# Kernel tuning notes

Hardware: AMD Instinct MI355X
Metric: run time of the kernel (lower is better)

## Reference

```python
import jax, jax.numpy as jnp
import numpy as np

TAU = 0.5
EPS = 1e-12  # torch F.normalize eps
N, HIDDEN, PROJ = 16384, 512, 128


def setup_inputs() -> dict:
    key = jax.random.key(0)
    k1, k2, k3, k4 = jax.random.split(key, 4)
    scale1 = 1.0 / np.sqrt(HIDDEN)
    scale2 = 1.0 / np.sqrt(PROJ)
    return {
        "z1": jax.random.normal(k1, (N, HIDDEN), dtype=jnp.float32),
        "z2": jax.random.normal(k2, (N, HIDDEN), dtype=jnp.float32),
        "W1": jax.random.normal(k3, (HIDDEN, PROJ), dtype=jnp.float32) * scale1,
        "b1": jnp.zeros((PROJ,), dtype=jnp.float32),
        "W2": jax.random.normal(k4, (PROJ, PROJ), dtype=jnp.float32) * scale2,
        "b2": jnp.zeros((PROJ,), dtype=jnp.float32),
    }


def _project(z, W1, b1, W2, b2):
    # GRACE projection head: Linear -> ELU -> Linear
    h = jax.nn.elu(z @ W1 + b1)
    return h @ W2 + b2


def _l2_normalize(x):
    nrm = jnp.sqrt(jnp.sum(x * x, axis=1, keepdims=True))
    return x / jnp.maximum(nrm, EPS)


def _semi_loss(u, v):
    nu = _l2_normalize(u)
    nv = _l2_normalize(v)
    intra = jnp.exp((nu @ nu.T) / TAU)  # [N, N]
    inter = jnp.exp((nu @ nv.T) / TAU)  # [N, N]
    pos = jnp.diagonal(inter)
    denom = intra.sum(axis=1) + inter.sum(axis=1) - jnp.diagonal(intra)
    return -jnp.log(pos / denom)


def reference(z1, z2, W1, b1, W2, b2):
    u = _project(z1, W1, b1, W2, b2)
    v = _project(z2, W1, b1, W2, b2)
    l1 = _semi_loss(u, v)
    l2 = _semi_loss(v, u)
    return jnp.mean((l1 + l2) * 0.5)
```

## Files before the change

### kernel.cpp

```cpp
#include <hip/hip_runtime.h>

#define NROWS 16384
#define M2    32768
#define TT    128
#define HID   512
#define PROJ  128

constexpr float SCALE_L2E = 2.8853900817779268f;
constexpr float E2        = 7.38905609893065f;

typedef float f32x2   __attribute__((ext_vector_type(2)));
typedef float f32x4   __attribute__((ext_vector_type(4)));
typedef short bf16x8  __attribute__((ext_vector_type(8)));
typedef int   i32x8   __attribute__((ext_vector_type(8)));

__device__ inline short f2bf(float x) {
  union { float f; unsigned u; } v; v.f = x;
  unsigned r = v.u + 0x7fffu + ((v.u >> 16) & 1u);
  return (short)(r >> 16);
}
__device__ inline float bf2f(short s) {
  union { unsigned u; float f; } v; v.u = ((unsigned)(unsigned short)s) << 16;
  return v.f;
}
__device__ inline unsigned char f2fp8(float x) {
  return (unsigned char)(__builtin_amdgcn_cvt_pk_fp8_f32(x, x, 0, false) & 0xff);
}
__device__ inline unsigned cvtpk_bf16(float a, float b) {
  unsigned r;
  asm("v_cvt_pk_bf16_f32 %0, %1, %2" : "=v"(r) : "v"(a), "v"(b));
  return r;
}

__global__ void kprep(const float* __restrict__ W1, const float* __restrict__ W2,
                      short* __restrict__ W1t, short* __restrict__ W2t) {
  int stride = gridDim.x * blockDim.x;
  for (int idx = blockIdx.x * blockDim.x + threadIdx.x; idx < 128 * 512; idx += stride) {
    int n = idx >> 9, k = idx & 511;
    W1t[idx] = f2bf(W1[k * 128 + n]);
  }
  for (int idx = blockIdx.x * blockDim.x + threadIdx.x; idx < 128 * 128; idx += stride) {
    int n = idx >> 7, k = idx & 127;
    W2t[idx] = f2bf(W2[k * 128 + n]);
  }
}

__global__ __launch_bounds__(256) void kproj1(const float* __restrict__ z1,
                                              const float* __restrict__ z2,
                                              const short* __restrict__ W1t,
                                              const float* __restrict__ b1,
                                              short* __restrict__ h) {
  int wave = threadIdx.x >> 6, lane = threadIdx.x & 63;
  int lr = lane & 15, lg = lane >> 4;
  const float* z = (blockIdx.x < 256) ? z1 : z2;
  int rloc = (blockIdx.x & 255) * 64 + wave * 16;
  int rglob0 = blockIdx.x * 64 + wave * 16;
  const float* zrow = z + (size_t)(rloc + lr) * HID;

  f32x4 acc[8];
#pragma unroll
  for (int ct = 0; ct < 8; ++ct) acc[ct] = (f32x4){0.f, 0.f, 0.f, 0.f};

  for (int kc = 0; kc < HID / 32; ++kc) {
    int kof = kc * 32 + lg * 8;
    f32x4 za = *(const f32x4*)(zrow + kof);
    f32x4 zb = *(const f32x4*)(zrow + kof + 4);
    union { unsigned u[4]; bf16x8 v; } af;
    af.u[0] = cvtpk_bf16(za[0], za[1]);
    af.u[1] = cvtpk_bf16(za[2], za[3]);
    af.u[2] = cvtpk_bf16(zb[0], zb[1]);
    af.u[3] = cvtpk_bf16(zb[2], zb[3]);
#pragma unroll
    for (int ct = 0; ct < 8; ++ct) {
      bf16x8 b = *(const bf16x8*)(W1t + (ct * 16 + lr) * HID + kof);
      acc[ct] = __builtin_amdgcn_mfma_f32_16x16x32_bf16(af.v, b, acc[ct], 0, 0, 0);
    }
  }
#pragma unroll
  for (int ct = 0; ct < 8; ++ct) {
    int col = ct * 16 + lr;
    float bias = b1[col];
#pragma unroll
    for (int q = 0; q < 4; ++q) {
      int row = rglob0 + lg * 4 + q;
      float x = acc[ct][q] + bias;
      x = x > 0.f ? x : expm1f(x);
      h[(size_t)row * PROJ + col] = f2bf(x);
    }
  }
}

__global__ __launch_bounds__(256) void kproj2(const short* __restrict__ h,
                                              const short* __restrict__ W2t,
                                              const float* __restrict__ b2,
                                              short* __restrict__ nn,
                                              unsigned char* __restrict__ nnf,
                                              unsigned char* __restrict__ nsf) {
  int wave = threadIdx.x >> 6, lane = threadIdx.x & 63;
  int lr = lane & 15, lg = lane >> 4;
  int row0 = blockIdx.x * 64 + wave * 16;
  const short* hrow = h + (size_t)(row0 + lr) * PROJ;

  f32x4 acc[8];
#pragma unroll
  for (int ct = 0; ct < 8; ++ct) acc[ct] = (f32x4){0.f, 0.f, 0.f, 0.f};

#pragma unroll
  for (int kc = 0; kc < PROJ / 32; ++kc) {
    int kof = kc * 32 + lg * 8;
    bf16x8 a = *(const bf16x8*)(hrow + kof);
#pragma unroll
    for (int ct = 0; ct < 8; ++ct) {
      bf16x8 b = *(const bf16x8*)(W2t + (ct * 16 + lr) * PROJ + kof);
      acc[ct] = __builtin_amdgcn_mfma_f32_16x16x32_bf16(a, b, acc[ct], 0, 0, 0);
    }
  }
#pragma unroll
  for (int ct = 0; ct < 8; ++ct) {
    float bias = b2[ct * 16 + lr];
#pragma unroll
    for (int q = 0; q < 4; ++q) acc[ct][q] += bias;
  }
  float inv[4];
#pragma unroll
  for (int q = 0; q < 4; ++q) {
    float s = 0.f;
#pragma unroll
    for (int ct = 0; ct < 8; ++ct) s += acc[ct][q] * acc[ct][q];
    s += __shfl_xor(s, 1); s += __shfl_xor(s, 2);
    s += __shfl_xor(s, 4); s += __shfl_xor(s, 8);
    inv[q] = 1.f / fmaxf(sqrtf(s), 1e-12f);
  }
#pragma unroll
  for (int ct = 0; ct < 8; ++ct) {
    int col = ct * 16 + lr;
#pragma unroll
    for (int q = 0; q < 4; ++q) {
      int row = row0 + lg * 4 + q;
      float v = acc[ct][q] * inv[q];
      nn[(size_t)row * PROJ + col]  = f2bf(v);
      nnf[(size_t)row * PROJ + col] = f2fp8(v);
      nsf[(size_t)row * PROJ + col] = f2fp8(v * SCALE_L2E);
    }
  }
}

__global__ __launch_bounds__(512, 4) void ksim11(const unsigned char* __restrict__ nnf,
                                                 const unsigned char* __restrict__ nsf,
                                                 float* __restrict__ d) {
  __shared__ long BtL[256 * 16];
  __shared__ float colbuf[8][256];

  int tid = threadIdx.x;
  int w = tid >> 6, lane = tid & 63;
  int lr = lane & 15, lg = lane >> 4;

  int t = blockIdx.x;
  float ff = (float)((2 * TT + 1) * (2 * TT + 1) - 8 * t);
  int ib = (int)(((float)(2 * TT + 1) - sqrtf(ff)) * 0.5f);
  if (ib < 0) ib = 0;
  if (ib > TT - 1) ib = TT - 1;
  while (ib > 0 && ib * (2 * TT - ib + 1) / 2 > t) --ib;
  while ((ib + 1) * (2 * TT - ib) / 2 <= t) ++ib;
  int jb = ib + (t - ib * (2 * TT - ib + 1) / 2);
  bool diag = (ib == jb);

  int i0 = ib * 256 + w * 32;

  i32x8 a[2];
#pragma unroll
  for (int rb = 0; rb < 2; ++rb)
    a[rb] = *(const i32x8*)(nsf + (size_t)(i0 + rb * 16 + lr) * PROJ + lg * 32);

  {
    int slot = tid & 15, row0 = tid >> 4;
    const long* bsrc = (const long*)(nnf + (size_t)(jb * 256 + row0) * PROJ) + slot;
    long st[8];
#pragma unroll
    for (int r = 0; r < 8; ++r) st[r] = bsrc[(size_t)r * 32 * 16];
#pragma unroll
    for (int r = 0; r < 8; ++r) {
      int row = r * 32 + row0;
      BtL[row * 16 + (slot ^ (row & 15))] = st[r];
    }
  }
  __syncthreads();

  f32x4 rs0 = (f32x4){0.f, 0.f, 0.f, 0.f};
  f32x4 rs1 = (f32x4){0.f, 0.f, 0.f, 0.f};

  const char* bb = (const char*)BtL + lr * 128;
  unsigned xo0 = (unsigned)(((lg * 4 + 0) ^ lr) << 3);
  unsigned xo1 = (unsigned)(((lg * 4 + 1) ^ lr) << 3);
  unsigned xo2 = (unsigned)(((lg * 4 + 2) ^ lr) << 3);
  unsigned xo3 = (unsigned)(((lg * 4 + 3) ^ lr) << 3);

  union BFrag { long h[4]; i32x8 v; };

  BFrag cur;
  cur.h[0] = *(const long*)(bb + xo0);
  cur.h[1] = *(const long*)(bb + xo1);
  cur.h[2] = *(const long*)(bb + xo2);
  cur.h[3] = *(const long*)(bb + xo3);

#pragma unroll 2
  for (int jt = 0; jt < 16; ++jt) {
    const char* bn = bb + 2048;
    BFrag nxt;
    nxt.h[0] = *(const long*)(bn + xo0);
    nxt.h[1] = *(const long*)(bn + xo1);
    nxt.h[2] = *(const long*)(bn + xo2);
    nxt.h[3] = *(const long*)(bn + xo3);

    f32x4 c0 = (f32x4){0.f, 0.f, 0.f, 0.f};
    f32x4 c1 = (f32x4){0.f, 0.f, 0.f, 0.f};
    c0 = __builtin_amdgcn_mfma_scale_f32_16x16x128_f8f6f4(a[0], cur.v, c0, 0, 0,
                                                          0, 0x7f7f7f7f, 0, 0x7f7f7f7f);
    c1 = __builtin_amdgcn_mfma_scale_f32_16x16x128_f8f6f4(a[1], cur.v, c1, 0, 0,
                                                          0, 0x7f7f7f7f, 0, 0x7f7f7f7f);

    f32x4 e0, e1;
#pragma unroll
    for (int q = 0; q < 4; ++q) {
      e0[q] = __builtin_amdgcn_exp2f(c0[q]);
      e1[q] = __builtin_amdgcn_exp2f(c1[q]);
    }
    rs0 += e0;
    rs1 += e1;
    f32x4 s4 = e0 + e1;
    f32x2 h2 = __builtin_shufflevector(s4, s4, 0, 1)
             + __builtin_shufflevector(s4, s4, 2, 3);
    float cs = h2[0] + h2[1];
    cs += __shfl_xor(cs, 16);
    cs += __shfl_xor(cs, 32);
    if (lg == 0) colbuf[w][jt * 16 + lr] = cs;

    cur = nxt;
    bb = bn;
  }

  float myval = 0.f;
#pragma unroll
  for (int rb = 0; rb < 2; ++rb)
#pragma unroll
    for (int q = 0; q < 4; ++q) {
      float v = (rb == 0) ? rs0[q] : rs1[q];
      v += __shfl_xor(v, 1); v += __shfl_xor(v, 2);
      v += __shfl_xor(v, 4); v += __shfl_xor(v, 8);
      if (lr == rb * 4 + q) myval = v;
    }
  if (lr < 8)
    atomicAdd(&d[i0 + (lr >> 2) * 16 + lg * 4 + (lr & 3)], myval);

  __syncthreads();
  if (!diag && tid < 256) {
    float s = 0.f;
#pragma unroll
    for (int w2 = 0; w2 < 8; ++w2) s += colbuf[w2][tid];
    atomicAdd(&d[jb * 256 + tid], s);
  }
}

__global__ __launch_bounds__(256) void kfinal(const short* __restrict__ nn,
                                              const float* __restrict__ d,
                                              float* __restrict__ out) {
  int wave = threadIdx.x >> 6, lane = threadIdx.x & 63;
  int i = blockIdx.x * 256 + threadIdx.x;

  const bf16x8* a = (const bf16x8*)(nn + (size_t)i * PROJ);
  const bf16x8* b = (const bf16x8*)(nn + (size_t)(NROWS + i) * PROJ);
  float s = 0.f;
#pragma unroll
  for (int t = 0; t < PROJ / 8; ++t) {
    bf16x8 x = a[t], y = b[t];
#pragma unroll
    for (int e = 0; e < 8; ++e) s += bf2f(x[e]) * bf2f(y[e]);
  }
  float den1 = d[i] - E2;
  float den2 = d[NROWS + i] - E2;
  float li = 0.5f * (logf(den1) + logf(den2)) - s * 2.0f;

#pragma unroll
  for (int m = 1; m < 64; m <<= 1) li += __shfl_xor(li, m);
  __shared__ float ws4[4];
  if (lane == 0) ws4[wave] = li;
  __syncthreads();
  if (threadIdx.x == 0)
    atomicAdd(out, (ws4[0] + ws4[1] + ws4[2] + ws4[3]) * (1.f / (float)NROWS));
}

extern "C" void kernel_launch(void* const* d_in, const int* in_sizes, int n_in,
                              void* d_out, int out_size, void* d_ws, size_t ws_size,
                              hipStream_t stream) {
  (void)in_sizes; (void)n_in; (void)out_size; (void)ws_size;
  const float* z1 = (const float*)d_in[0];
  const float* z2 = (const float*)d_in[1];
  const float* W1 = (const float*)d_in[2];
  const float* b1 = (const float*)d_in[3];
  const float* W2 = (const float*)d_in[4];
  const float* b2 = (const float*)d_in[5];
  float* out = (float*)d_out;

  short* W1t = (short*)d_ws;
  short* W2t = W1t + 128 * 512;
  short* hb  = W2t + 128 * 128;
  short* nn  = hb  + (size_t)M2 * PROJ;
  unsigned char* nnf = (unsigned char*)(nn + (size_t)M2 * PROJ);
  unsigned char* nsf = nnf + (size_t)M2 * PROJ;
  float* d = (float*)(nsf + (size_t)M2 * PROJ);

  hipMemsetAsync(d_out, 0, sizeof(float), stream);
  hipMemsetAsync(d, 0, (size_t)M2 * sizeof(float), stream);

  kprep<<<16, 256, 0, stream>>>(W1, W2, W1t, W2t);
  kproj1<<<M2 / 64, 256, 0, stream>>>(z1, z2, W1t, b1, hb);
  kproj2<<<M2 / 64, 256, 0, stream>>>(hb, W2t, b2, nn, nnf, nsf);
  ksim11<<<TT * (TT + 1) / 2, 512, 0, stream>>>(nnf, nsf, d);
  kfinal<<<NROWS / 256, 256, 0, stream>>>(nn, d, out);
}
```

Before: 189.1 us.

## Fuse projection kernels via LDS and interleave two column streams in sim loop

Merges the two projection GEMM kernels into one, passing the ELU hidden tile through swizzled shared memory instead of a global bf16 buffer, which removes one launch and the global round trip of the hidden activations. The similarity kernel's inner loop now processes two independent column tiles (first and second half) per iteration, doubling MFMA/exp2 independence per step to improve instruction-level parallelism. This raises register pressure in the sim kernel and adds 16KB of LDS per projection block.

```diff
diff --git a/kernel.cpp b/kernel.cpp
--- a/kernel.cpp
+++ b/kernel.cpp
@@ -45,11 +45,16 @@
   }
 }
 
-__global__ __launch_bounds__(256) void kproj1(const float* __restrict__ z1,
-                                              const float* __restrict__ z2,
-                                              const short* __restrict__ W1t,
-                                              const float* __restrict__ b1,
-                                              short* __restrict__ h) {
+__global__ __launch_bounds__(256) void kproj(const float* __restrict__ z1,
+                                             const float* __restrict__ z2,
+                                             const short* __restrict__ W1t,
+                                             const float* __restrict__ b1,
+                                             const short* __restrict__ W2t,
+                                             const float* __restrict__ b2,
+                                             short* __restrict__ nn,
+                                             unsigned char* __restrict__ nnf,
+                                             unsigned char* __restrict__ nsf) {
+  __shared__ short hls[64 * 128];
   int wave = threadIdx.x >> 6, lane = threadIdx.x & 63;
   int lr = lane & 15, lg = lane >> 4;
   const float* z = (blockIdx.x < 256) ? z1 : z2;
@@ -82,51 +87,41 @@
     float bias = b1[col];
 #pragma unroll
     for (int q = 0; q < 4; ++q) {
-      int row = rglob0 + lg * 4 + q;
+      int lrow = wave * 16 + lg * 4 + q;
       float x = acc[ct][q] + bias;
       x = x > 0.f ? x : expm1f(x);
-      h[(size_t)row * PROJ + col] = f2bf(x);
-    }
-  }
-}
-
-__global__ __launch_bounds__(256) void kproj2(const short* __restrict__ h,
-                                              const short* __restrict__ W2t,
-                                              const float* __restrict__ b2,
-                                              short* __restrict__ nn,
-                                              unsigned char* __restrict__ nnf,
-                                              unsigned char* __restrict__ nsf) {
-  int wave = threadIdx.x >> 6, lane = threadIdx.x & 63;
-  int lr = lane & 15, lg = lane >> 4;
-  int row0 = blockIdx.x * 64 + wave * 16;
-  const short* hrow = h + (size_t)(row0 + lr) * PROJ;
-
-  f32x4 acc[8];
-#pragma unroll
-  for (int ct = 0; ct < 8; ++ct) acc[ct] = (f32x4){0.f, 0.f, 0.f, 0.f};
+      int sw = (col >> 3) ^ (lrow & 15);
+      hls[lrow * 128 + sw * 8 + (col & 7)] = f2bf(x);
+    }
+  }
+  __syncthreads();
+
+  int lrow2 = wave * 16 + lr;
+  f32x4 acc2[8];
+#pragma unroll
+  for (int ct = 0; ct < 8; ++ct) acc2[ct] = (f32x4){0.f, 0.f, 0.f, 0.f};
 
 #pragma unroll
   for (int kc = 0; kc < PROJ / 32; ++kc) {
-    int kof = kc * 32 + lg * 8;
-    bf16x8 a = *(const bf16x8*)(hrow + kof);
+    bf16x8 a = *(const bf16x8*)&hls[lrow2 * 128 + (((kc * 4 + lg) ^ lr) << 3)];
 #pragma unroll
     for (int ct = 0; ct < 8; ++ct) {
-      bf16x8 b = *(const bf16x8*)(W2t + (ct * 16 + lr) * PROJ + kof);
-      acc[ct] = __builtin_amdgcn_mfma_f32_16x16x32_bf16(a, b, acc[ct], 0, 0, 0);
+      bf16x8 b = *(const bf16x8*)(W2t + (ct * 16 + lr) * PROJ + kc * 32 + lg * 8);
+      acc2[ct] = __builtin_amdgcn_mfma_f32_16x16x32_bf16(a, b, acc2[ct], 0, 0, 0);
     }
   }
 #pragma unroll
   for (int ct = 0; ct < 8; ++ct) {
     float bias = b2[ct * 16 + lr];
 #pragma unroll
-    for (int q = 0; q < 4; ++q) acc[ct][q] += bias;
+    for (int q = 0; q < 4; ++q) acc2[ct][q] += bias;
   }
   float inv[4];
 #pragma unroll
   for (int q = 0; q < 4; ++q) {
     float s = 0.f;
 #pragma unroll
-    for (int ct = 0; ct < 8; ++ct) s += acc[ct][q] * acc[ct][q];
+    for (int ct = 0; ct < 8; ++ct) s += acc2[ct][q] * acc2[ct][q];
     s += __shfl_xor(s, 1); s += __shfl_xor(s, 2);
     s += __shfl_xor(s, 4); s += __shfl_xor(s, 8);
     inv[q] = 1.f / fmaxf(sqrtf(s), 1e-12f);
@@ -136,8 +131,8 @@
     int col = ct * 16 + lr;
 #pragma unroll
     for (int q = 0; q < 4; ++q) {
-      int row = row0 + lg * 4 + q;
-      float v = acc[ct][q] * inv[q];
+      int row = rglob0 + lg * 4 + q;
+      float v = acc2[ct][q] * inv[q];
       nn[(size_t)row * PROJ + col]  = f2bf(v);
       nnf[(size_t)row * PROJ + col] = f2fp8(v);
       nsf[(size_t)row * PROJ + col] = f2fp8(v * SCALE_L2E);
@@ -145,7 +140,7 @@
   }
 }
 
-__global__ __launch_bounds__(512, 4) void ksim11(const unsigned char* __restrict__ nnf,
+__global__ __launch_bounds__(512, 4) void ksim12(const unsigned char* __restrict__ nnf,
                                                  const unsigned char* __restrict__ nsf,
                                                  float* __restrict__ d) {
   __shared__ long BtL[256 * 16];
@@ -167,10 +162,8 @@
 
   int i0 = ib * 256 + w * 32;
 
-  i32x8 a[2];
-#pragma unroll
-  for (int rb = 0; rb < 2; ++rb)
-    a[rb] = *(const i32x8*)(nsf + (size_t)(i0 + rb * 16 + lr) * PROJ + lg * 32);
+  i32x8 a0 = *(const i32x8*)(nsf + (size_t)(i0 + lr) * PROJ + lg * 32);
+  i32x8 a1 = *(const i32x8*)(nsf + (size_t)(i0 + 16 + lr) * PROJ + lg * 32);
 
   {
     int slot = tid & 15, row0 = tid >> 4;
@@ -189,7 +182,8 @@
   f32x4 rs0 = (f32x4){0.f, 0.f, 0.f, 0.f};
   f32x4 rs1 = (f32x4){0.f, 0.f, 0.f, 0.f};
 
-  const char* bb = (const char*)BtL + lr * 128;
+  const char* bbA = (const char*)BtL + lr * 128;
+  const char* bbB = bbA + 8 * 2048;
   unsigned xo0 = (unsigned)(((lg * 4 + 0) ^ lr) << 3);
   unsigned xo1 = (unsigned)(((lg * 4 + 1) ^ lr) << 3);
   unsigned xo2 = (unsigned)(((lg * 4 + 2) ^ lr) << 3);
@@ -197,46 +191,74 @@
 
   union BFrag { long h[4]; i32x8 v; };
 
-  BFrag cur;
-  cur.h[0] = *(const long*)(bb + xo0);
-  cur.h[1] = *(const long*)(bb + xo1);
-  cur.h[2] = *(const long*)(bb + xo2);
-  cur.h[3] = *(const long*)(bb + xo3);
+  BFrag curA, curB;
+  curA.h[0] = *(const long*)(bbA + xo0);
+  curA.h[1] = *(const long*)(bbA + xo1);
+  curA.h[2] = *(const long*)(bbA + xo2);
+  curA.h[3] = *(const long*)(bbA + xo3);
+  curB.h[0] = *(const long*)(bbB + xo0);
+  curB.h[1] = *(const long*)(bbB + xo1);
+  curB.h[2] = *(const long*)(bbB + xo2);
+  curB.h[3] = *(const long*)(bbB + xo3);
 
 #pragma unroll 2
-  for (int jt = 0; jt < 16; ++jt) {
-    const char* bn = bb + 2048;
-    BFrag nxt;
-    nxt.h[0] = *(const long*)(bn + xo0);
-    nxt.h[1] = *(const long*)(bn + xo1);
-    nxt.h[2] = *(const long*)(bn + xo2);
-    nxt.h[3] = *(const long*)(bn + xo3);
-
-    f32x4 c0 = (f32x4){0.f, 0.f, 0.f, 0.f};
-    f32x4 c1 = (f32x4){0.f, 0.f, 0.f, 0.f};
-    c0 = __builtin_amdgcn_mfma_scale_f32_16x16x128_f8f6f4(a[0], cur.v, c0, 0, 0,
-                                                          0, 0x7f7f7f7f, 0, 0x7f7f7f7f);
-    c1 = __builtin_amdgcn_mfma_scale_f32_16x16x128_f8f6f4(a[1], cur.v, c1, 0, 0,
-                                                          0, 0x7f7f7f7f, 0, 0x7f7f7f7f);
-
-    f32x4 e0, e1;
+  for (int jt = 0; jt < 8; ++jt) {
+    const char* bnA = bbA + 2048;
+    const char* bnB = bbB + 2048;
+    BFrag nxtA, nxtB;
+    nxtA.h[0] = *(const long*)(bnA + xo0);
+    nxtA.h[1] = *(const long*)(bnA + xo1);
+    nxtA.h[2] = *(const long*)(bnA + xo2);
+    nxtA.h[3] = *(const long*)(bnA + xo3);
+    nxtB.h[0] = *(const long*)(bnB + xo0);
+    nxtB.h[1] = *(const long*)(bnB + xo1);
+    nxtB.h[2] = *(const long*)(bnB + xo2);
+    nxtB.h[3] = *(const long*)(bnB + xo3);
+
+    f32x4 cA0 = (f32x4){0.f, 0.f, 0.f, 0.f};
+    f32x4 cA1 = (f32x4){0.f, 0.f, 0.f, 0.f};
+    f32x4 cB0 = (f32x4){0.f, 0.f, 0.f, 0.f};
+    f32x4 cB1 = (f32x4){0.f, 0.f, 0.f, 0.f};
+    cA0 = __builtin_amdgcn_mfma_scale_f32_16x16x128_f8f6f4(a0, curA.v, cA0, 0, 0,
+                                                           0, 0x7f7f7f7f, 0, 0x7f7f7f7f);
+    cA1 = __builtin_amdgcn_mfma_scale_f32_16x16x128_f8f6f4(a1, curA.v, cA1, 0, 0,
+                                                           0, 0x7f7f7f7f, 0, 0x7f7f7f7f);
+    cB0 = __builtin_amdgcn_mfma_scale_f32_16x16x128_f8f6f4(a0, curB.v, cB0, 0, 0,
+                                                           0, 0x7f7f7f7f, 0, 0x7f7f7f7f);
+    cB1 = __builtin_amdgcn_mfma_scale_f32_16x16x128_f8f6f4(a1, curB.v, cB1, 0, 0,
+                                                           0, 0x7f7f7f7f, 0, 0x7f7f7f7f);
+
 #pragma unroll
     for (int q = 0; q < 4; ++q) {
-      e0[q] = __builtin_amdgcn_exp2f(c0[q]);
-      e1[q] = __builtin_amdgcn_exp2f(c1[q]);
-    }
-    rs0 += e0;
-    rs1 += e1;
-    f32x4 s4 = e0 + e1;
-    f32x2 h2 = __builtin_shufflevector(s4, s4, 0, 1)
-             + __builtin_shufflevector(s4, s4, 2, 3);
-    float cs = h2[0] + h2[1];
-    cs += __shfl_xor(cs, 16);
-    cs += __shfl_xor(cs, 32);
-    if (lg == 0) colbuf[w][jt * 16 + lr] = cs;
-
-    cur = nxt;
-    bb = bn;
+      cA0[q] = __builtin_amdgcn_exp2f(cA0[q]);
+      cA1[q] = __builtin_amdgcn_exp2f(cA1[q]);
+      cB0[q] = __builtin_amdgcn_exp2f(cB0[q]);
+      cB1[q] = __builtin_amdgcn_exp2f(cB1[q]);
+    }
+    rs0 += cA0; rs1 += cA1;
+    rs0 += cB0; rs1 += cB1;
+
+    f32x4 sA = cA0 + cA1;
+    f32x2 hA = __builtin_shufflevector(sA, sA, 0, 1)
+             + __builtin_shufflevector(sA, sA, 2, 3);
+    float csA = hA[0] + hA[1];
+    csA += __shfl_xor(csA, 16);
+    csA += __shfl_xor(csA, 32);
+
+    f32x4 sB = cB0 + cB1;
+    f32x2 hB = __builtin_shufflevector(sB, sB, 0, 1)
+             + __builtin_shufflevector(sB, sB, 2, 3);
+    float csB = hB[0] + hB[1];
+    csB += __shfl_xor(csB, 16);
+    csB += __shfl_xor(csB, 32);
+
+    if (lg == 0) {
+      colbuf[w][jt * 16 + lr]        = csA;
+      colbuf[w][(jt + 8) * 16 + lr]  = csB;
+    }
+
+    curA = nxtA; curB = nxtB;
+    bbA = bnA; bbB = bnB;
   }
 
   float myval = 0.f;
@@ -303,8 +325,7 @@
 
   short* W1t = (short*)d_ws;
   short* W2t = W1t + 128 * 512;
-  short* hb  = W2t + 128 * 128;
-  short* nn  = hb  + (size_t)M2 * PROJ;
+  short* nn  = W2t + 128 * 128;
   unsigned char* nnf = (unsigned char*)(nn + (size_t)M2 * PROJ);
   unsigned char* nsf = nnf + (size_t)M2 * PROJ;
   float* d = (float*)(nsf + (size_t)M2 * PROJ);
@@ -313,8 +334,7 @@
   hipMemsetAsync(d, 0, (size_t)M2 * sizeof(float), stream);
 
   kprep<<<16, 256, 0, stream>>>(W1, W2, W1t, W2t);
-  kproj1<<<M2 / 64, 256, 0, stream>>>(z1, z2, W1t, b1, hb);
-  kproj2<<<M2 / 64, 256, 0, stream>>>(hb, W2t, b2, nn, nnf, nsf);
-  ksim11<<<TT * (TT + 1) / 2, 512, 0, stream>>>(nnf, nsf, d);
+  kproj<<<M2 / 64, 256, 0, stream>>>(z1, z2, W1t, b1, W2t, b2, nn, nnf, nsf);
+  ksim12<<<TT * (TT + 1) / 2, 512, 0, stream>>>(nnf, nsf, d);
   kfinal<<<NROWS / 256, 256, 0, stream>>>(nn, d, out);
 }
```

New measurement: 204.2 us. +8.0%, slower.
